# Performance work log

Measured on AMD Instinct MI355X. Metric: run time of the kernel, lower is better.

The kernel has to match this reference:

```python
import jax, jax.numpy as jnp
import numpy as np

N_EMBD = 448
HEAD_SIZE = 64

def setup_inputs() -> dict:
    key = jax.random.key(0)
    k1, k2, k3, k4 = jax.random.split(key, 4)
    B, T = 16, 2048
    x = jax.random.normal(k1, (B, T, N_EMBD), dtype=jnp.float32)
    # nn.Linear(n_embd, head_size, bias=False): weight shape (head_size, n_embd); y = x @ W.T
    s = 1.0 / np.sqrt(N_EMBD)
    Wk = jax.random.uniform(k2, (HEAD_SIZE, N_EMBD), jnp.float32, -s, s)
    Wq = jax.random.uniform(k3, (HEAD_SIZE, N_EMBD), jnp.float32, -s, s)
    Wv = jax.random.uniform(k4, (HEAD_SIZE, N_EMBD), jnp.float32, -s, s)
    return {"x": x, "Wk": Wk, "Wq": Wq, "Wv": Wv}

def reference(x, Wk, Wq, Wv):
    B, T, C = x.shape
    k = jnp.einsum('btc,hc->bth', x, Wk)  # (B,T,H)
    q = jnp.einsum('btc,hc->bth', x, Wq)
    v = jnp.einsum('btc,hc->bth', x, Wv)
    scale = 1.0 / jnp.sqrt(jnp.float32(C))  # NOTE: scales by sqrt(n_embd), as in source
    wei = jnp.einsum('bth,bsh->bts', q, k) * scale  # (B,T,T)
    causal = jnp.tril(jnp.ones((T, T), dtype=bool))
    wei = jnp.where(causal[None, :, :], wei, -jnp.inf)
    wei = jax.nn.softmax(wei, axis=-1)
    # dropout is identity in eval mode
    out = jnp.einsum('bts,bsh->bth', wei, v)  # (B,T,H)
    return out
```

## Files before the change

### kernel.cpp

```cpp
#include <hip/hip_runtime.h>
#include <math.h>

#define BT 32768
#define NC 448
#define NH 64
#define TT 2048

typedef __bf16 bf16x8 __attribute__((ext_vector_type(8)));
typedef float  f32x4  __attribute__((ext_vector_type(4)));

__device__ __forceinline__ unsigned short f2bf(float f) {
  unsigned u = __builtin_bit_cast(unsigned, f);
  return (unsigned short)((u + 0x7FFFu + ((u >> 16) & 1u)) >> 16);
}
__device__ __forceinline__ ushort4 f2bf4(float4 v) {
  ushort4 b; b.x = f2bf(v.x); b.y = f2bf(v.y); b.z = f2bf(v.z); b.w = f2bf(v.w);
  return b;
}


__global__ __launch_bounds__(256) void proj_kernel(
    const float* __restrict__ x, const float* __restrict__ Wk,
    const float* __restrict__ Wq, const float* __restrict__ Wv,
    unsigned short* __restrict__ kws, unsigned short* __restrict__ qws,
    unsigned short* __restrict__ vws)
{
  __shared__ unsigned short xs[2][4096];
  __shared__ unsigned short wsm[2][4096];
  const int tid = threadIdx.x;
  const int w = tid >> 6, lane = tid & 63;
  const int q = lane >> 4, l15 = lane & 15;
  const int r0 = blockIdx.x * 64;
  const int p = blockIdx.y;
  const float* W = (p == 0) ? Wk : ((p == 1) ? Wq : Wv);

  f32x4 acc[4];
#pragma unroll
  for (int i = 0; i < 4; ++i) acc[i] = f32x4{0.f, 0.f, 0.f, 0.f};

  const int c0 = (tid & 15) * 4, r_ = tid >> 4;

  float4 xr[4], wr[4];
#pragma unroll
  for (int i = 0; i < 4; ++i) {
    xr[i] = *(const float4*)&x[(size_t)(r0 + r_ + 16 * i) * NC + c0];
    wr[i] = *(const float4*)&W[(size_t)(r_ + 16 * i) * NC + c0];
  }

  for (int ch = 0; ch < 7; ++ch) {
    const int cur = ch & 1;
#pragma unroll
    for (int i = 0; i < 4; ++i) {
      int r = r_ + 16 * i;
      int off = r * 64 + (((c0 >> 3) ^ (r & 7)) << 3) + (c0 & 7);
      *(ushort4*)&xs[cur][off]  = f2bf4(xr[i]);
      *(ushort4*)&wsm[cur][off] = f2bf4(wr[i]);
    }
    __syncthreads();
    if (ch < 6) {
      int kc = (ch + 1) * 64;
#pragma unroll
      for (int i = 0; i < 4; ++i) {
        xr[i] = *(const float4*)&x[(size_t)(r0 + r_ + 16 * i) * NC + kc + c0];
        wr[i] = *(const float4*)&W[(size_t)(r_ + 16 * i) * NC + kc + c0];
      }
    }
#pragma unroll
    for (int ks = 0; ks < 2; ++ks) {
      int xrow = w * 16 + l15;
      int g = q + 4 * ks;
      bf16x8 xf = *(const bf16x8*)&xs[cur][xrow * 64 + ((g ^ (xrow & 7)) << 3)];
#pragma unroll
      for (int t = 0; t < 4; ++t) {
        int wrow = t * 16 + l15;
        bf16x8 wf = *(const bf16x8*)&wsm[cur][wrow * 64 + ((g ^ (wrow & 7)) << 3)];
        if (p == 0)
          acc[t] = __builtin_amdgcn_mfma_f32_16x16x32_bf16(wf, xf, acc[t], 0, 0, 0);
        else
          acc[t] = __builtin_amdgcn_mfma_f32_16x16x32_bf16(xf, wf, acc[t], 0, 0, 0);
      }
    }
  }

  const size_t tile = (size_t)blockIdx.x * 4096;
  if (p == 0) {
#pragma unroll
    for (int t = 0; t < 4; ++t) {
      int j = w * 16 + l15;
      ushort4 bb; bb.x = f2bf(acc[t][0]); bb.y = f2bf(acc[t][1]);
      bb.z = f2bf(acc[t][2]); bb.w = f2bf(acc[t][3]);
      *(ushort4*)&kws[tile + j * 64 + (((2 * t + (q >> 1)) ^ (j & 7)) << 3) + ((q & 1) << 2)] = bb;
    }
  } else if (p == 1) {
    const float qs = 0.068161075f;
#pragma unroll
    for (int t = 0; t < 4; ++t) {
      int h = t * 16 + l15;
#pragma unroll
      for (int rr = 0; rr < 4; ++rr) {
        int R = r0 + w * 16 + q * 4 + rr;
        qws[(size_t)R * 64 + h] = f2bf(acc[t][rr] * qs);
      }
    }
  } else {
#pragma unroll
    for (int t = 0; t < 4; ++t) {
      int h = t * 16 + l15;
      ushort4 bb; bb.x = f2bf(acc[t][0]); bb.y = f2bf(acc[t][1]);
      bb.z = f2bf(acc[t][2]); bb.w = f2bf(acc[t][3]);
      *(ushort4*)&vws[tile + h * 64 + (((2 * w + (q >> 1)) ^ (h & 7)) << 3) + ((q & 1) << 2)] = bb;
    }
  }
}

__global__ __launch_bounds__(256) void attn_kernel(
    const unsigned short* __restrict__ kws, const unsigned short* __restrict__ qws,
    const unsigned short* __restrict__ vws, float* __restrict__ out)
{
  __shared__ unsigned short ksm[2][4096];
  __shared__ unsigned short vtm[2][4096];
  __shared__ unsigned short psm[4096];
  const int qt = 31 - (int)blockIdx.x, b = blockIdx.y;
  const int tid = threadIdx.x;
  const int w = tid >> 6, lane = tid & 63;
  const int q = lane >> 4, l15 = lane & 15;
  const int t0 = b * TT + qt * 64;
  const int l7 = l15 & 7;

  bf16x8 qf[2];
#pragma unroll
  for (int ks = 0; ks < 2; ++ks)
    qf[ks] = *(const bf16x8*)&qws[(size_t)(t0 + w * 16 + l15) * 64 + 32 * ks + q * 8];

  f32x4 oacc[4];
#pragma unroll
  for (int ht = 0; ht < 4; ++ht) oacc[ht] = f32x4{0.f, 0.f, 0.f, 0.f};
  float m_i = -INFINITY, l_i = 0.f;

  uint4 kr0, kr1, vr0, vr1;
  {
    const unsigned short* kt_ = kws + (size_t)(b * 32 + 0) * 4096;
    const unsigned short* vt_ = vws + (size_t)(b * 32 + 0) * 4096;
    kr0 = *(const uint4*)&kt_[tid * 8];  kr1 = *(const uint4*)&kt_[2048 + tid * 8];
    vr0 = *(const uint4*)&vt_[tid * 8];  vr1 = *(const uint4*)&vt_[2048 + tid * 8];
  }

  for (int kt = 0; kt <= qt; ++kt) {
    const int cur = kt & 1;
    *(uint4*)&ksm[cur][tid * 8] = kr0;  *(uint4*)&ksm[cur][2048 + tid * 8] = kr1;
    *(uint4*)&vtm[cur][tid * 8] = vr0;  *(uint4*)&vtm[cur][2048 + tid * 8] = vr1;
    __syncthreads();
    if (kt < qt) {
      const unsigned short* kt_ = kws + (size_t)(b * 32 + kt + 1) * 4096;
      const unsigned short* vt_ = vws + (size_t)(b * 32 + kt + 1) * 4096;
      kr0 = *(const uint4*)&kt_[tid * 8];  kr1 = *(const uint4*)&kt_[2048 + tid * 8];
      vr0 = *(const uint4*)&vt_[tid * 8];  vr1 = *(const uint4*)&vt_[2048 + tid * 8];
    }

    f32x4 sacc[4];
#pragma unroll
    for (int jt = 0; jt < 4; ++jt) sacc[jt] = f32x4{0.f, 0.f, 0.f, 0.f};
#pragma unroll
    for (int jt = 0; jt < 4; ++jt) {
      int j = jt * 16 + l15;
#pragma unroll
      for (int ks = 0; ks < 2; ++ks) {
        bf16x8 kf = *(const bf16x8*)&ksm[cur][j * 64 + (((q + 4 * ks) ^ (j & 7)) << 3)];
        sacc[jt] = __builtin_amdgcn_mfma_f32_16x16x32_bf16(kf, qf[ks], sacc[jt], 0, 0, 0);
      }
    }

    if (kt == qt) {
      int iloc = w * 16 + l15;
#pragma unroll
      for (int jt = 0; jt < 4; ++jt)
#pragma unroll
        for (int rr = 0; rr < 4; ++rr)
          if (jt * 16 + q * 4 + rr > iloc) sacc[jt][rr] = -INFINITY;
    }

    float mx = -INFINITY;
#pragma unroll
    for (int jt = 0; jt < 4; ++jt)
#pragma unroll
      for (int rr = 0; rr < 4; ++rr) mx = fmaxf(mx, sacc[jt][rr]);
    mx = fmaxf(mx, __shfl_xor(mx, 16));
    mx = fmaxf(mx, __shfl_xor(mx, 32));
    float mn = fmaxf(m_i, mx);
    float alpha = exp2f(m_i - mn);
    m_i = mn;
    float p[4][4], rs = 0.f;
#pragma unroll
    for (int jt = 0; jt < 4; ++jt)
#pragma unroll
      for (int rr = 0; rr < 4; ++rr) {
        float pv = exp2f(sacc[jt][rr] - mn);
        p[jt][rr] = pv; rs += pv;
      }
    rs += __shfl_xor(rs, 16);
    rs += __shfl_xor(rs, 32);
    l_i = l_i * alpha + rs;

    float a_t[4];
#pragma unroll
    for (int rr = 0; rr < 4; ++rr) a_t[rr] = __shfl(alpha, q * 4 + rr);
#pragma unroll
    for (int ht = 0; ht < 4; ++ht)
#pragma unroll
      for (int rr = 0; rr < 4; ++rr) oacc[ht][rr] *= a_t[rr];

    {
      int row = w * 16 + l15;
#pragma unroll
      for (int jt = 0; jt < 4; ++jt) {
        ushort4 bb; bb.x = f2bf(p[jt][0]); bb.y = f2bf(p[jt][1]);
        bb.z = f2bf(p[jt][2]); bb.w = f2bf(p[jt][3]);
        *(ushort4*)&psm[row * 64 + (((2 * jt + (q >> 1)) ^ l7) << 3) + ((q & 1) << 2)] = bb;
      }
    }

#pragma unroll
    for (int ks2 = 0; ks2 < 2; ++ks2) {
      int prow = w * 16 + l15;
      bf16x8 pf = *(const bf16x8*)&psm[prow * 64 + (((q + 4 * ks2) ^ l7) << 3)];
#pragma unroll
      for (int ht = 0; ht < 4; ++ht) {
        int h = ht * 16 + l15;
        bf16x8 vf = *(const bf16x8*)&vtm[cur][h * 64 + (((q + 4 * ks2) ^ l7) << 3)];
        oacc[ht] = __builtin_amdgcn_mfma_f32_16x16x32_bf16(pf, vf, oacc[ht], 0, 0, 0);
      }
    }
  }

  float l_t[4];
#pragma unroll
  for (int rr = 0; rr < 4; ++rr) l_t[rr] = __shfl(l_i, q * 4 + rr);
#pragma unroll
  for (int rr = 0; rr < 4; ++rr) {
    float inv = 1.f / l_t[rr];
    int R = t0 + w * 16 + q * 4 + rr;
#pragma unroll
    for (int ht = 0; ht < 4; ++ht)
      out[(size_t)R * 64 + ht * 16 + l15] = oacc[ht][rr] * inv;
  }
}

extern "C" void kernel_launch(void* const* d_in, const int* in_sizes, int n_in,
                              void* d_out, int out_size, void* d_ws, size_t ws_size,
                              hipStream_t stream) {
  const float* x  = (const float*)d_in[0];
  const float* Wk = (const float*)d_in[1];
  const float* Wq = (const float*)d_in[2];
  const float* Wv = (const float*)d_in[3];
  unsigned short* kws = (unsigned short*)d_ws;
  unsigned short* qws = kws + (size_t)BT * NH;
  unsigned short* vws = qws + (size_t)BT * NH;
  float* out = (float*)d_out;

  proj_kernel<<<dim3(512, 3), 256, 0, stream>>>(x, Wk, Wq, Wv, kws, qws, vws);
  attn_kernel<<<dim3(32, 16), 256, 0, stream>>>(kws, qws, vws, out);
}
```

Baseline: 156.9 us.

## Split long causal attention rows into two KV chunks with a combine pass

```diff
diff --git a/kernel.cpp b/kernel.cpp
--- a/kernel.cpp
+++ b/kernel.cpp
@@ -113,14 +113,21 @@
   }
 }
 
-__global__ __launch_bounds__(256) void attn_kernel(
+__global__ __launch_bounds__(256) void attn_partial(
     const unsigned short* __restrict__ kws, const unsigned short* __restrict__ qws,
-    const unsigned short* __restrict__ vws, float* __restrict__ out)
+    const unsigned short* __restrict__ vws, float* __restrict__ out,
+    float* __restrict__ opart, float* __restrict__ mlpart)
 {
   __shared__ unsigned short ksm[2][4096];
   __shared__ unsigned short vtm[2][4096];
   __shared__ unsigned short psm[4096];
-  const int qt = 31 - (int)blockIdx.x, b = blockIdx.y;
+  const int bx = blockIdx.x, b = blockIdx.y;
+  int qt, kt0, ktn, ci; bool direct;
+  if (bx < 16)      { qt = 16 + bx; kt0 = 0;  ktn = 16;     ci = 0; direct = false; }
+  else if (bx < 32) { qt = 47 - bx; kt0 = 16; ktn = qt + 1; ci = 1; direct = false; }
+  else              { qt = 47 - bx; kt0 = 0;  ktn = qt + 1; ci = 0; direct = true;  }
+  const int nt = ktn - kt0;
+
   const int tid = threadIdx.x;
   const int w = tid >> 6, lane = tid & 63;
   const int q = lane >> 4, l15 = lane & 15;
@@ -139,18 +146,19 @@
 
   uint4 kr0, kr1, vr0, vr1;
   {
-    const unsigned short* kt_ = kws + (size_t)(b * 32 + 0) * 4096;
-    const unsigned short* vt_ = vws + (size_t)(b * 32 + 0) * 4096;
+    const unsigned short* kt_ = kws + (size_t)(b * 32 + kt0) * 4096;
+    const unsigned short* vt_ = vws + (size_t)(b * 32 + kt0) * 4096;
     kr0 = *(const uint4*)&kt_[tid * 8];  kr1 = *(const uint4*)&kt_[2048 + tid * 8];
     vr0 = *(const uint4*)&vt_[tid * 8];  vr1 = *(const uint4*)&vt_[2048 + tid * 8];
   }
 
-  for (int kt = 0; kt <= qt; ++kt) {
-    const int cur = kt & 1;
+  for (int it = 0; it < nt; ++it) {
+    const int kt = kt0 + it;
+    const int cur = it & 1;
     *(uint4*)&ksm[cur][tid * 8] = kr0;  *(uint4*)&ksm[cur][2048 + tid * 8] = kr1;
     *(uint4*)&vtm[cur][tid * 8] = vr0;  *(uint4*)&vtm[cur][2048 + tid * 8] = vr1;
     __syncthreads();
-    if (kt < qt) {
+    if (it + 1 < nt) {
       const unsigned short* kt_ = kws + (size_t)(b * 32 + kt + 1) * 4096;
       const unsigned short* vt_ = vws + (size_t)(b * 32 + kt + 1) * 4096;
       kr0 = *(const uint4*)&kt_[tid * 8];  kr1 = *(const uint4*)&kt_[2048 + tid * 8];
@@ -232,16 +240,63 @@
     }
   }
 
-  float l_t[4];
-#pragma unroll
-  for (int rr = 0; rr < 4; ++rr) l_t[rr] = __shfl(l_i, q * 4 + rr);
-#pragma unroll
-  for (int rr = 0; rr < 4; ++rr) {
-    float inv = 1.f / l_t[rr];
-    int R = t0 + w * 16 + q * 4 + rr;
-#pragma unroll
-    for (int ht = 0; ht < 4; ++ht)
-      out[(size_t)R * 64 + ht * 16 + l15] = oacc[ht][rr] * inv;
+  if (direct) {
+    float l_t[4];
+#pragma unroll
+    for (int rr = 0; rr < 4; ++rr) l_t[rr] = __shfl(l_i, q * 4 + rr);
+#pragma unroll
+    for (int rr = 0; rr < 4; ++rr) {
+      float inv = 1.f / l_t[rr];
+      int R = t0 + w * 16 + q * 4 + rr;
+#pragma unroll
+      for (int ht = 0; ht < 4; ++ht)
+        out[(size_t)R * 64 + ht * 16 + l15] = oacc[ht][rr] * inv;
+    }
+  } else {
+    const size_t slot = (size_t)(b * 16 + (qt - 16)) * 2 + ci;
+    float* Op = opart + slot * 4096;
+#pragma unroll
+    for (int rr = 0; rr < 4; ++rr) {
+      int rloc = w * 16 + q * 4 + rr;
+#pragma unroll
+      for (int ht = 0; ht < 4; ++ht)
+        Op[rloc * 64 + ht * 16 + l15] = oacc[ht][rr];
+    }
+    if (q == 0) {
+      mlpart[slot * 128 + w * 16 + l15]      = m_i;
+      mlpart[slot * 128 + 64 + w * 16 + l15] = l_i;
+    }
+  }
+}
+
+__global__ __launch_bounds__(256) void combine_kernel(
+    const float* __restrict__ opart, const float* __restrict__ mlpart,
+    float* __restrict__ out)
+{
+  const int qtc = blockIdx.x, b = blockIdx.y;
+  const int qt = 16 + qtc;
+  const int t = threadIdx.x;
+  const int r = t >> 2, c0 = (t & 3) * 16;
+  const size_t s0 = (size_t)(b * 16 + qtc) * 2;
+
+  float m0 = mlpart[s0 * 128 + r],       l0 = mlpart[s0 * 128 + 64 + r];
+  float m1 = mlpart[(s0 + 1) * 128 + r], l1 = mlpart[(s0 + 1) * 128 + 64 + r];
+  float m  = fmaxf(m0, m1);
+  float w0 = exp2f(m0 - m), w1 = exp2f(m1 - m);
+  float inv = 1.f / (w0 * l0 + w1 * l1);
+  w0 *= inv; w1 *= inv;
+
+  const float* O0 = opart + s0 * 4096 + r * 64;
+  const float* O1 = opart + (s0 + 1) * 4096 + r * 64;
+  float* op = out + (size_t)(b * TT + qt * 64 + r) * 64;
+#pragma unroll
+  for (int j = 0; j < 4; ++j) {
+    float4 a  = *(const float4*)&O0[c0 + j * 4];
+    float4 bb = *(const float4*)&O1[c0 + j * 4];
+    float4 o;
+    o.x = w0 * a.x + w1 * bb.x;  o.y = w0 * a.y + w1 * bb.y;
+    o.z = w0 * a.z + w1 * bb.z;  o.w = w0 * a.w + w1 * bb.w;
+    *(float4*)&op[c0 + j * 4] = o;
   }
 }
 
@@ -255,8 +310,11 @@
   unsigned short* kws = (unsigned short*)d_ws;
   unsigned short* qws = kws + (size_t)BT * NH;
   unsigned short* vws = qws + (size_t)BT * NH;
+  float* opart  = (float*)(vws + (size_t)BT * NH);
+  float* mlpart = opart + (size_t)512 * 4096;
   float* out = (float*)d_out;
 
   proj_kernel<<<dim3(512, 3), 256, 0, stream>>>(x, Wk, Wq, Wv, kws, qws, vws);
-  attn_kernel<<<dim3(32, 16), 256, 0, stream>>>(kws, qws, vws, out);
-}
+  attn_partial<<<dim3(48, 16), 256, 0, stream>>>(kws, qws, vws, out, opart, mlpart);
+  combine_kernel<<<dim3(16, 16), 256, 0, stream>>>(opart, mlpart, out);
+}
```

Measured after the change: 147.1 us. 6.2% less time.
